# Kernel tuning notes

Measured on AMD Instinct MI355X. Metric: run time of the kernel, lower is better.

## Reference

```python
import jax, jax.numpy as jnp
import numpy as np

N = 100_000   # total nodes in batched graph
E = 1_600_000 # total edges (avg degree 16)
G = 64        # graphs in batch
DIMS = [1, 128, 128, 128]


def setup_inputs() -> dict:
    key = jax.random.key(0)
    ks = jax.random.split(key, 12)
    src = jax.random.randint(ks[0], (E,), 0, N, dtype=jnp.int32)
    dst = jax.random.randint(ks[1], (E,), 0, N, dtype=jnp.int32)
    graph_ids = jnp.sort(jax.random.randint(ks[2], (N,), 0, G, dtype=jnp.int32))
    inp = {"src": src, "dst": dst, "graph_ids": graph_ids}
    # GraphConv weights (glorot-ish scale) and biases
    for i in range(len(DIMS) - 1):
        fan = DIMS[i] + DIMS[i + 1]
        inp[f"W{i+1}"] = jax.random.normal(ks[3 + 2 * i], (DIMS[i], DIMS[i + 1]), jnp.float32) * jnp.sqrt(2.0 / fan)
        inp[f"b{i+1}"] = jnp.zeros((DIMS[i + 1],), jnp.float32)
    inp["Wc"] = jax.random.normal(ks[10], (DIMS[-1], 2), jnp.float32) * 0.1
    inp["bc"] = jnp.zeros((2,), jnp.float32)
    return inp


def reference(src, dst, graph_ids, W1, b1, W2, b2, W3, b3, Wc, bc):
    ones_e = jnp.ones((E,), jnp.float32)
    deg_in = jax.ops.segment_sum(ones_e, dst, num_segments=N)   # [N]
    deg_out = jax.ops.segment_sum(ones_e, src, num_segments=N)  # [N]
    # DGL GraphConv norm='both': clamp degrees to >=1
    norm_src = jnp.clip(deg_out, 1.0, None) ** -0.5  # [N]
    norm_dst = jnp.clip(deg_in, 1.0, None) ** -0.5   # [N]

    h = deg_in[:, None]  # node feature = in-degree, [N,1]
    for W, b in ((W1, b1), (W2, b2), (W3, b3)):
        msg = (h * norm_src[:, None])[src]                       # [E,d] gather
        agg = jax.ops.segment_sum(msg, dst, num_segments=N)      # [N,d] scatter-add
        h = jax.nn.relu((agg * norm_dst[:, None]) @ W + b)       # [N,d_out]

    # dgl.mean_nodes: per-graph mean of node features
    counts = jax.ops.segment_sum(jnp.ones((N,), jnp.float32), graph_ids, num_segments=G)
    hg = jax.ops.segment_sum(h, graph_ids, num_segments=G) / jnp.clip(counts, 1.0, None)[:, None]  # [G,d]
    return hg @ Wc + bc  # [G,2]
```

## Files before the change

### kernel.cpp

```cpp
#include <hip/hip_runtime.h>
#include <hip/hip_fp8.h>


#define DHID 128
#define NGRAPH 64
#define CAPSH 6
#define SPAN 12500
#define NR 8
#define HB 32
#define PB 1024

typedef float floatx2 __attribute__((ext_vector_type(2)));

__device__ __forceinline__ unsigned int ftof8(float f) {
  __hip_fp8_e4m3 t(f);
  return (unsigned int)t.__x;
}

__device__ __forceinline__ void fma4(float4& a, float s, const float4& w) {
  a.x = fmaf(s, w.x, a.x);
  a.y = fmaf(s, w.y, a.y);
  a.z = fmaf(s, w.z, a.z);
  a.w = fmaf(s, w.w, a.w);
}

__device__ __forceinline__ void dec8(uint2 v, float* acc) {
  floatx2 f0 = __builtin_amdgcn_cvt_pk_f32_fp8((int)v.x, false);
  floatx2 f1 = __builtin_amdgcn_cvt_pk_f32_fp8((int)v.x, true);
  floatx2 f2 = __builtin_amdgcn_cvt_pk_f32_fp8((int)v.y, false);
  floatx2 f3 = __builtin_amdgcn_cvt_pk_f32_fp8((int)v.y, true);
  acc[0] += f0.x; acc[1] += f0.y;
  acc[2] += f1.x; acc[3] += f1.y;
  acc[4] += f2.x; acc[5] += f2.y;
  acc[6] += f3.x; acc[7] += f3.y;
}

__global__ __launch_bounds__(256) void k_phist(
    const int* __restrict__ src, const int* __restrict__ dst,
    int* __restrict__ pcnt_d, int* __restrict__ pcnt_s, int E) {
  __shared__ int cd[NR], cs[NR];
  const int tid = threadIdx.x, b = blockIdx.x;
  if (tid < NR) { cd[tid] = 0; cs[tid] = 0; }
  __syncthreads();
  const int per = (E + PB - 1) / PB;
  const int e1 = min(b * per + per, E);
  for (int e = b * per + tid; e < e1; e += 256) {
    atomicAdd(&cd[dst[e] / SPAN], 1);
    atomicAdd(&cs[src[e] / SPAN], 1);
  }
  __syncthreads();
  if (tid < NR) {
    pcnt_d[b * NR + tid] = cd[tid];
    pcnt_s[b * NR + tid] = cs[tid];
  }
}

__global__ __launch_bounds__(1024) void k_pscan(int* __restrict__ pcnt,
                                                int* __restrict__ bstart, int E) {
  __shared__ int wsum[16];
  const int tid = threadIdx.x;
  const int lane = tid & 63, wave = tid >> 6;
  int v[8], s = 0;
#pragma unroll
  for (int j = 0; j < 8; ++j) {
    int idx = tid * 8 + j;
    int q = idx >> 10, b = idx & (PB - 1);
    v[j] = pcnt[b * NR + q];
    s += v[j];
  }
  int incl = s;
#pragma unroll
  for (int d = 1; d < 64; d <<= 1) {
    int u = __shfl_up(incl, d, 64);
    if (lane >= d) incl += u;
  }
  if (lane == 63) wsum[wave] = incl;
  __syncthreads();
  if (tid < 16) {
    int x = wsum[tid];
#pragma unroll
    for (int d = 1; d < 16; d <<= 1) {
      int u = __shfl_up(x, d, 16);
      if (tid >= d) x += u;
    }
    wsum[tid] = x;
  }
  __syncthreads();
  int base = (wave ? wsum[wave - 1] : 0) + (incl - s);
#pragma unroll
  for (int j = 0; j < 8; ++j) {
    int idx = tid * 8 + j;
    int q = idx >> 10, b = idx & (PB - 1);
    pcnt[b * NR + q] = base;
    if (b == 0) bstart[q] = base;
    base += v[j];
  }
  if (tid == 1023) bstart[NR] = E;
}

__global__ __launch_bounds__(256) void k_ppart(
    const int* __restrict__ src, const int* __restrict__ dst,
    const int* __restrict__ pcnt_d, const int* __restrict__ pcnt_s,
    int* __restrict__ bsrc, int* __restrict__ bdst, int* __restrict__ ssrc, int E) {
  __shared__ int cd[NR], cs[NR];
  const int tid = threadIdx.x, b = blockIdx.x;
  if (tid < NR) {
    cd[tid] = pcnt_d[b * NR + tid];
    cs[tid] = pcnt_s[b * NR + tid];
  }
  __syncthreads();
  const int per = (E + PB - 1) / PB;
  const int e1 = min(b * per + per, E);
  for (int e = b * per + tid; e < e1; e += 256) {
    int d = dst[e], s = src[e];
    int pd_ = atomicAdd(&cd[d / SPAN], 1);
    bdst[pd_] = d;
    bsrc[pd_] = s;
    int ps_ = atomicAdd(&cs[s / SPAN], 1);
    ssrc[ps_] = s;
  }
}

__global__ __launch_bounds__(256) void k_histb(const int* __restrict__ key,
                                               const int* __restrict__ bstart,
                                               int* __restrict__ partial) {
  __shared__ int lh[SPAN];
  const int b = blockIdx.x, q = blockIdx.y, tid = threadIdx.x;
  const int lo = q * SPAN;
  for (int i = tid; i < SPAN; i += 256) lh[i] = 0;
  __syncthreads();
  const int s0 = bstart[q];
  const int cnt = bstart[q + 1] - s0;
  const int per = (cnt + HB - 1) / HB;
  const int e0 = s0 + b * per;
  const int e1 = min(e0 + per, s0 + cnt);
  for (int e = e0 + tid; e < e1; e += 256) {
    unsigned r = (unsigned)(key[e] - lo);
    if (r < SPAN) atomicAdd(&lh[r], 1);
  }
  __syncthreads();
  int* gp = partial + ((size_t)(q * HB + b)) * SPAN;
  for (int i = tid; i < SPAN; i += 256) gp[i] = lh[i];
}

__global__ __launch_bounds__(256) void k_scan(
    int* __restrict__ pd, const int* __restrict__ ps, const int* __restrict__ gid,
    int* __restrict__ degin, int* __restrict__ degout, float* __restrict__ nodeval,
    float* __restrict__ countsF, int N) {
  __shared__ float lcounts[NGRAPH];
  const int tid = threadIdx.x;
  const int n = blockIdx.x * 256 + tid;
  if (tid < NGRAPH) lcounts[tid] = 0.0f;
  __syncthreads();
  if (n < N) {
    int q = n / SPAN, r = n - q * SPAN;
    size_t col = (size_t)(q * HB) * SPAN + r;
    int running = n << CAPSH;
    int dout = 0;
#pragma unroll 8
    for (int b = 0; b < HB; ++b) {
      size_t idx = col + (size_t)b * SPAN;
      int c = pd[idx];
      pd[idx] = running;
      running += c;
      dout += ps[idx];
    }
    int di = min(running - (n << CAPSH), 1 << CAPSH);
    degin[n] = di;
    degout[n] = dout;
    nodeval[n] = (float)di * rsqrtf(fmaxf((float)dout, 1.0f));
    atomicAdd(&lcounts[gid[n]], 1.0f);
  }
  __syncthreads();
  if (tid < NGRAPH) {
    float c = lcounts[tid];
    if (c != 0.0f) atomicAdd(&countsF[tid], c);
  }
}

__global__ __launch_bounds__(256) void k_placeb(
    const int* __restrict__ bsrc, const int* __restrict__ bdst,
    const int* __restrict__ bstart, const int* __restrict__ base,
    int* __restrict__ eidx) {
  __shared__ int lc[SPAN];
  const int b = blockIdx.x, q = blockIdx.y, tid = threadIdx.x;
  const int lo = q * SPAN;
  const int* bp = base + ((size_t)(q * HB + b)) * SPAN;
  for (int i = tid; i < SPAN; i += 256) lc[i] = bp[i];
  __syncthreads();
  const int s0 = bstart[q];
  const int cnt = bstart[q + 1] - s0;
  const int per = (cnt + HB - 1) / HB;
  const int e0 = s0 + b * per;
  const int e1 = min(e0 + per, s0 + cnt);
  for (int e = e0 + tid; e < e1; e += 256) {
    int d = bdst[e];
    unsigned r = (unsigned)(d - lo);
    if (r < SPAN) {
      int pos = atomicAdd(&lc[r], 1);
      if (pos < ((d + 1) << CAPSH)) eidx[pos] = bsrc[e];
    }
  }
}

__global__ __launch_bounds__(256) void k_l1(
    const float* __restrict__ nodeval, const int* __restrict__ degin,
    const int* __restrict__ degout, const int* __restrict__ eidx,
    const float* __restrict__ W1, const float* __restrict__ b1,
    unsigned char* __restrict__ hA, int N) {
  __shared__ float xa[256];
  __shared__ float xs[256];
  const int tid = threadIdx.x;
  const int n0 = blockIdx.x * 256;
  const int n = n0 + tid;
  if (n < N) {
    int o = n << CAPSH, c = degin[n];
    float acc = 0.0f;
    for (int i = 0; i < c; ++i) acc += nodeval[eidx[o + i]];
    xa[tid] = acc * rsqrtf(fmaxf((float)c, 1.0f));
    xs[tid] = rsqrtf(fmaxf((float)degout[n], 1.0f));
  } else {
    xa[tid] = 0.0f;
    xs[tid] = 0.0f;
  }
  __syncthreads();
  const int nlim = min(256, N - n0);
#pragma unroll 4
  for (int it = 0; it < 16; ++it) {
    int slot = it * 256 + tid;
    int ln = slot >> 4, ch = slot & 15;
    if (ln >= nlim) break;
    float x = xa[ln], ns = xs[ln];
    unsigned lo = 0, hi = 0;
#pragma unroll
    for (int j = 0; j < 4; ++j) {
      float v = fmaxf(fmaf(x, W1[ch * 8 + j], b1[ch * 8 + j]), 0.0f) * ns;
      lo |= ftof8(v) << (8 * j);
    }
#pragma unroll
    for (int j = 0; j < 4; ++j) {
      float v = fmaxf(fmaf(x, W1[ch * 8 + 4 + j], b1[ch * 8 + 4 + j]), 0.0f) * ns;
      hi |= ftof8(v) << (8 * j);
    }
    *(uint2*)(hA + (size_t)(n0 + ln) * DHID + ch * 8) = make_uint2(lo, hi);
  }
}

template <int MODE>
__global__ __launch_bounds__(256) void k_agg_mm(
    const unsigned char* __restrict__ hs, const int* __restrict__ degin,
    const int* __restrict__ degout, const int* __restrict__ eidx,
    const float* __restrict__ W, const float* __restrict__ bias,
    unsigned char* __restrict__ hOut, const int* __restrict__ gid,
    float* __restrict__ hg, int N) {
  __shared__ float xl[32][DHID];
  const int tid = threadIdx.x;
  const int base = blockIdx.x * 32;
  const int g16 = tid >> 4;
  const int l16 = tid & 15;

#pragma unroll
  for (int rep = 0; rep < 2; ++rep) {
    int n = g16 + rep * 16;
    int node = base + n;
    float acc[8] = {0.f, 0.f, 0.f, 0.f, 0.f, 0.f, 0.f, 0.f};
    if (node < N) {
      int o = node << CAPSH, c = degin[node];
      const unsigned char* hp = hs + l16 * 8;
      int i = 0;
      for (; i + 3 < c; i += 4) {
        int s0 = eidx[o + i + 0];
        int s1 = eidx[o + i + 1];
        int s2 = eidx[o + i + 2];
        int s3 = eidx[o + i + 3];
        uint2 v0 = *(const uint2*)(hp + ((size_t)s0 << 7));
        uint2 v1 = *(const uint2*)(hp + ((size_t)s1 << 7));
        uint2 v2 = *(const uint2*)(hp + ((size_t)s2 << 7));
        uint2 v3 = *(const uint2*)(hp + ((size_t)s3 << 7));
        dec8(v0, acc);
        dec8(v1, acc);
        dec8(v2, acc);
        dec8(v3, acc);
      }
      for (; i < c; ++i) {
        uint2 v = *(const uint2*)(hp + ((size_t)eidx[o + i] << 7));
        dec8(v, acc);
      }
      float nd = rsqrtf(fmaxf((float)c, 1.0f));
#pragma unroll
      for (int j = 0; j < 8; ++j) acc[j] *= nd;
    }
    *((float4*)&xl[n][l16 * 8]) = make_float4(acc[0], acc[1], acc[2], acc[3]);
    *((float4*)&xl[n][l16 * 8 + 4]) = make_float4(acc[4], acc[5], acc[6], acc[7]);
  }
  __syncthreads();

  const int jg = tid & 31;
  const int ng = tid >> 5;
  const float* wj = W + jg * 4;

  float4 acc[4];
#pragma unroll
  for (int i = 0; i < 4; ++i) acc[i] = make_float4(0.f, 0.f, 0.f, 0.f);

#pragma unroll 4
  for (int k = 0; k < DHID; k += 4) {
    float4 w0 = *(const float4*)(wj + (size_t)(k + 0) * DHID);
    float4 w1 = *(const float4*)(wj + (size_t)(k + 1) * DHID);
    float4 w2 = *(const float4*)(wj + (size_t)(k + 2) * DHID);
    float4 w3 = *(const float4*)(wj + (size_t)(k + 3) * DHID);
#pragma unroll
    for (int i = 0; i < 4; ++i) {
      float4 x = *(const float4*)&xl[ng * 4 + i][k];
      fma4(acc[i], x.x, w0);
      fma4(acc[i], x.y, w1);
      fma4(acc[i], x.z, w2);
      fma4(acc[i], x.w, w3);
    }
  }

  float4 bb = *(const float4*)(bias + jg * 4);

  if (MODE == 0) {
#pragma unroll
    for (int i = 0; i < 4; ++i) {
      int node = base + ng * 4 + i;
      if (node < N) {
        float ns = rsqrtf(fmaxf((float)degout[node], 1.0f));
        unsigned int w = 0;
        w |= ftof8(fmaxf(acc[i].x + bb.x, 0.0f) * ns);
        w |= ftof8(fmaxf(acc[i].y + bb.y, 0.0f) * ns) << 8;
        w |= ftof8(fmaxf(acc[i].z + bb.z, 0.0f) * ns) << 16;
        w |= ftof8(fmaxf(acc[i].w + bb.w, 0.0f) * ns) << 24;
        *(unsigned int*)(hOut + (size_t)node * DHID + jg * 4) = w;
      }
    }
  } else {
    __syncthreads();
#pragma unroll
    for (int i = 0; i < 4; ++i) {
      int n = ng * 4 + i;
      float4 r;
      r.x = fmaxf(acc[i].x + bb.x, 0.0f);
      r.y = fmaxf(acc[i].y + bb.y, 0.0f);
      r.z = fmaxf(acc[i].z + bb.z, 0.0f);
      r.w = fmaxf(acc[i].w + bb.w, 0.0f);
      *((float4*)&xl[n][0] + jg) = r;
    }
    __syncthreads();
    if (tid < DHID) {
      float s = 0.0f;
      int gcur = gid[base];
      for (int n = 0; n < 32; ++n) {
        int node = base + n;
        if (node >= N) break;
        int g = gid[node];
        if (g != gcur) {
          atomicAdd(&hg[gcur * DHID + tid], s);
          s = 0.0f;
          gcur = g;
        }
        s += xl[n][tid];
      }
      atomicAdd(&hg[gcur * DHID + tid], s);
    }
  }
}

__global__ void k_out(const float* __restrict__ hg, const float* __restrict__ countsF,
                      const float* __restrict__ Wc, const float* __restrict__ bc,
                      float* __restrict__ out) {
  int t = threadIdx.x;
  int g = t >> 1, c = t & 1;
  float acc = 0.0f;
  for (int d = 0; d < DHID; ++d) acc = fmaf(hg[g * DHID + d], Wc[d * 2 + c], acc);
  out[t] = acc / fmaxf(countsF[g], 1.0f) + bc[c];
}

extern "C" void kernel_launch(void* const* d_in, const int* in_sizes, int n_in,
                              void* d_out, int out_size, void* d_ws, size_t ws_size,
                              hipStream_t stream) {
  const int* src = (const int*)d_in[0];
  const int* dst = (const int*)d_in[1];
  const int* gid = (const int*)d_in[2];
  const float* W1 = (const float*)d_in[3];
  const float* b1 = (const float*)d_in[4];
  const float* W2 = (const float*)d_in[5];
  const float* b2 = (const float*)d_in[6];
  const float* W3 = (const float*)d_in[7];
  const float* b3 = (const float*)d_in[8];
  const float* Wc = (const float*)d_in[9];
  const float* bc = (const float*)d_in[10];
  float* out = (float*)d_out;
  const int E = in_sizes[0];
  const int N = in_sizes[2];
  const int NBLK = (N + 255) / 256;

  char* ws = (char*)d_ws;
  size_t o = 0;
  auto alloc = [&](size_t bytes) {
    void* p = ws + o;
    o += (bytes + 255) & ~(size_t)255;
    return p;
  };
  unsigned char* hA = (unsigned char*)alloc((size_t)N * DHID);
  unsigned char* hB = (unsigned char*)alloc((size_t)N * DHID);
  int* eidx = (int*)alloc(((size_t)N << CAPSH) * 4);
  int* pd = (int*)alloc((size_t)NR * HB * SPAN * 4);
  int* ps = (int*)alloc((size_t)NR * HB * SPAN * 4);
  int* bsrc = (int*)alloc((size_t)E * 4);
  int* bdst = (int*)alloc((size_t)E * 4);
  int* ssrc = (int*)alloc((size_t)E * 4);
  int* pcnt_d = (int*)alloc((size_t)PB * NR * 4);
  int* pcnt_s = (int*)alloc((size_t)PB * NR * 4);
  int* bstart_d = (int*)alloc((NR + 1) * 4);
  int* bstart_s = (int*)alloc((NR + 1) * 4);
  size_t z0 = o;
  float* hg = (float*)alloc((size_t)NGRAPH * DHID * 4);
  float* countsF = (float*)alloc((size_t)NGRAPH * 4);
  size_t z1 = o;
  int* degin = (int*)alloc((size_t)N * 4);
  int* degout = (int*)alloc((size_t)N * 4);
  float* nodeval = (float*)alloc((size_t)N * 4);
  (void)ws_size;

  hipMemsetAsync(ws + z0, 0, z1 - z0, stream);

  k_phist<<<PB, 256, 0, stream>>>(src, dst, pcnt_d, pcnt_s, E);
  k_pscan<<<1, 1024, 0, stream>>>(pcnt_d, bstart_d, E);
  k_pscan<<<1, 1024, 0, stream>>>(pcnt_s, bstart_s, E);
  k_ppart<<<PB, 256, 0, stream>>>(src, dst, pcnt_d, pcnt_s, bsrc, bdst, ssrc, E);
  k_histb<<<dim3(HB, NR), 256, 0, stream>>>(bdst, bstart_d, pd);
  k_histb<<<dim3(HB, NR), 256, 0, stream>>>(ssrc, bstart_s, ps);
  k_scan<<<NBLK, 256, 0, stream>>>(pd, ps, gid, degin, degout, nodeval, countsF, N);
  k_placeb<<<dim3(HB, NR), 256, 0, stream>>>(bsrc, bdst, bstart_d, pd, eidx);
  k_l1<<<NBLK, 256, 0, stream>>>(nodeval, degin, degout, eidx, W1, b1, hA, N);
  k_agg_mm<0><<<(N + 31) / 32, 256, 0, stream>>>(hA, degin, degout, eidx, W2, b2, hB, gid, hg, N);
  k_agg_mm<1><<<(N + 31) / 32, 256, 0, stream>>>(hB, degin, degout, eidx, W3, b3, nullptr, gid, hg, N);
  k_out<<<1, 128, 0, stream>>>(hg, countsF, Wc, bc, out);
}
```

Before: 301.8 us.

## Repartition edges into 64 small node ranges and merge the two prefix scans

Changes the two-level partitioning to 64 node ranges of 1563 nodes with 8 histogram blocks each and 256 partition blocks. The smaller per-range shared histograms should raise occupancy of k_histb and k_placeb, and the k_scan column loop shrinks to 8 steps. The partition counts are stored range-major so the prefix scan reads them contiguously, and the two scans now run as one two-block launch. The layer-1 gather also reads edge indices as int4 to issue four independent loads at once, at the cost of more shared-memory atomics per partition block.

```diff
diff --git a/kernel.cpp b/kernel.cpp
--- a/kernel.cpp
+++ b/kernel.cpp
@@ -5,10 +5,10 @@
 #define DHID 128
 #define NGRAPH 64
 #define CAPSH 6
-#define SPAN 12500
-#define NR 8
-#define HB 32
-#define PB 1024
+#define SPAN 1563
+#define NR 64
+#define HB 8
+#define PB 256
 
 typedef float floatx2 __attribute__((ext_vector_type(2)));
 
@@ -50,24 +50,23 @@
   }
   __syncthreads();
   if (tid < NR) {
-    pcnt_d[b * NR + tid] = cd[tid];
-    pcnt_s[b * NR + tid] = cs[tid];
-  }
-}
-
-__global__ __launch_bounds__(1024) void k_pscan(int* __restrict__ pcnt,
-                                                int* __restrict__ bstart, int E) {
+    pcnt_d[tid * PB + b] = cd[tid];
+    pcnt_s[tid * PB + b] = cs[tid];
+  }
+}
+
+__global__ __launch_bounds__(1024) void k_pscan(
+    int* __restrict__ pcnt_d, int* __restrict__ bstart_d,
+    int* __restrict__ pcnt_s, int* __restrict__ bstart_s, int E) {
+  int* pcnt = blockIdx.x ? pcnt_s : pcnt_d;
+  int* bstart = blockIdx.x ? bstart_s : bstart_d;
   __shared__ int wsum[16];
   const int tid = threadIdx.x;
   const int lane = tid & 63, wave = tid >> 6;
-  int v[8], s = 0;
-#pragma unroll
-  for (int j = 0; j < 8; ++j) {
-    int idx = tid * 8 + j;
-    int q = idx >> 10, b = idx & (PB - 1);
-    v[j] = pcnt[b * NR + q];
-    s += v[j];
-  }
+  const int e0 = tid * 16;
+  int s = 0;
+#pragma unroll
+  for (int j = 0; j < 16; ++j) s += pcnt[e0 + j];
   int incl = s;
 #pragma unroll
   for (int d = 1; d < 64; d <<= 1) {
@@ -86,16 +85,16 @@
     wsum[tid] = x;
   }
   __syncthreads();
-  int base = (wave ? wsum[wave - 1] : 0) + (incl - s);
-#pragma unroll
-  for (int j = 0; j < 8; ++j) {
-    int idx = tid * 8 + j;
-    int q = idx >> 10, b = idx & (PB - 1);
-    pcnt[b * NR + q] = base;
-    if (b == 0) bstart[q] = base;
-    base += v[j];
-  }
-  if (tid == 1023) bstart[NR] = E;
+  int run = (wave ? wsum[wave - 1] : 0) + (incl - s);
+#pragma unroll
+  for (int j = 0; j < 16; ++j) {
+    int idx = e0 + j;
+    int c = pcnt[idx];
+    pcnt[idx] = run;
+    if ((idx & (PB - 1)) == 0) bstart[idx >> 8] = run;
+    run += c;
+  }
+  if (tid == 0) bstart[NR] = E;
 }
 
 __global__ __launch_bounds__(256) void k_ppart(
@@ -105,8 +104,8 @@
   __shared__ int cd[NR], cs[NR];
   const int tid = threadIdx.x, b = blockIdx.x;
   if (tid < NR) {
-    cd[tid] = pcnt_d[b * NR + tid];
-    cs[tid] = pcnt_s[b * NR + tid];
+    cd[tid] = pcnt_d[tid * PB + b];
+    cs[tid] = pcnt_s[tid * PB + b];
   }
   __syncthreads();
   const int per = (E + PB - 1) / PB;
@@ -157,7 +156,7 @@
     size_t col = (size_t)(q * HB) * SPAN + r;
     int running = n << CAPSH;
     int dout = 0;
-#pragma unroll 8
+#pragma unroll
     for (int b = 0; b < HB; ++b) {
       size_t idx = col + (size_t)b * SPAN;
       int c = pd[idx];
@@ -216,7 +215,16 @@
   if (n < N) {
     int o = n << CAPSH, c = degin[n];
     float acc = 0.0f;
-    for (int i = 0; i < c; ++i) acc += nodeval[eidx[o + i]];
+    int i = 0;
+    for (; i + 3 < c; i += 4) {
+      int4 e4 = *(const int4*)(eidx + o + i);
+      float v0 = nodeval[e4.x];
+      float v1 = nodeval[e4.y];
+      float v2 = nodeval[e4.z];
+      float v3 = nodeval[e4.w];
+      acc += (v0 + v1) + (v2 + v3);
+    }
+    for (; i < c; ++i) acc += nodeval[eidx[o + i]];
     xa[tid] = acc * rsqrtf(fmaxf((float)c, 1.0f));
     xs[tid] = rsqrtf(fmaxf((float)degout[n], 1.0f));
   } else {
@@ -411,8 +419,8 @@
   int* bsrc = (int*)alloc((size_t)E * 4);
   int* bdst = (int*)alloc((size_t)E * 4);
   int* ssrc = (int*)alloc((size_t)E * 4);
-  int* pcnt_d = (int*)alloc((size_t)PB * NR * 4);
-  int* pcnt_s = (int*)alloc((size_t)PB * NR * 4);
+  int* pcnt_d = (int*)alloc((size_t)NR * PB * 4);
+  int* pcnt_s = (int*)alloc((size_t)NR * PB * 4);
   int* bstart_d = (int*)alloc((NR + 1) * 4);
   int* bstart_s = (int*)alloc((NR + 1) * 4);
   size_t z0 = o;
@@ -427,8 +435,7 @@
   hipMemsetAsync(ws + z0, 0, z1 - z0, stream);
 
   k_phist<<<PB, 256, 0, stream>>>(src, dst, pcnt_d, pcnt_s, E);
-  k_pscan<<<1, 1024, 0, stream>>>(pcnt_d, bstart_d, E);
-  k_pscan<<<1, 1024, 0, stream>>>(pcnt_s, bstart_s, E);
+  k_pscan<<<2, 1024, 0, stream>>>(pcnt_d, bstart_d, pcnt_s, bstart_s, E);
   k_ppart<<<PB, 256, 0, stream>>>(src, dst, pcnt_d, pcnt_s, bsrc, bdst, ssrc, E);
   k_histb<<<dim3(HB, NR), 256, 0, stream>>>(bdst, bstart_d, pd);
   k_histb<<<dim3(HB, NR), 256, 0, stream>>>(ssrc, bstart_s, ps);
```

Result: faster. 283.7 us (-6.0%).
